# Optimization experiments

Measured on AMD Instinct MI355X. Metric: run time of the kernel, lower is better.

## Reference

```python
import jax, jax.numpy as jnp
import numpy as np

B, T, I, H, L, C = 8192, 50, 50, 10, 3, 5


def setup_inputs() -> dict:
    key = jax.random.key(0)
    ks = jax.random.split(key, 20)
    s = 1.0 / np.sqrt(H)  # torch nn.RNN init scale
    inp = {
        "x": jax.random.normal(ks[0], (B, T, I), dtype=jnp.float32),
        "h0": jax.random.normal(ks[1], (L, B, H), dtype=jnp.float32),
    }
    # per-layer weights: layer 0 takes input_size I, layers 1,2 take H
    in_sizes = [I, H, H]
    for l in range(L):
        inp[f"W_ih{l}"] = jax.random.uniform(ks[2 + 4 * l], (H, in_sizes[l]), minval=-s, maxval=s, dtype=jnp.float32)
        inp[f"W_hh{l}"] = jax.random.uniform(ks[3 + 4 * l], (H, H), minval=-s, maxval=s, dtype=jnp.float32)
        inp[f"b_ih{l}"] = jax.random.uniform(ks[4 + 4 * l], (H,), minval=-s, maxval=s, dtype=jnp.float32)
        inp[f"b_hh{l}"] = jax.random.uniform(ks[5 + 4 * l], (H,), minval=-s, maxval=s, dtype=jnp.float32)
    sf = 1.0 / np.sqrt(H * T)
    inp["fc_w"] = jax.random.uniform(ks[14], (C, H * T), minval=-sf, maxval=sf, dtype=jnp.float32)
    inp["fc_b"] = jax.random.uniform(ks[15], (C,), minval=-sf, maxval=sf, dtype=jnp.float32)
    return inp


def _rnn_layer(x, h0, W_ih, b_ih, W_hh, b_hh):
    # x: [B, T, in], h0: [B, H]. h_t = tanh(x_t W_ih^T + b_ih + h_{t-1} W_hh^T + b_hh)
    xW = jnp.einsum("bti,hi->bth", x, W_ih) + (b_ih + b_hh)  # input proj precomputed

    def step(h, xw_t):
        h = jnp.tanh(xw_t + h @ W_hh.T)
        return h, h

    _, ys = jax.lax.scan(step, h0, jnp.swapaxes(xW, 0, 1))  # ys: [T, B, H]
    return jnp.swapaxes(ys, 0, 1)  # [B, T, H]


def reference(x, h0, W_ih0, W_hh0, b_ih0, b_hh0, W_ih1, W_hh1, b_ih1, b_hh1,
              W_ih2, W_hh2, b_ih2, b_hh2, fc_w, fc_b):
    layers = [(W_ih0, b_ih0, W_hh0, b_hh0),
              (W_ih1, b_ih1, W_hh1, b_hh1),
              (W_ih2, b_ih2, W_hh2, b_hh2)]
    out = x
    for l, (Wi, bi, Wh, bh) in enumerate(layers):
        out = _rnn_layer(out, h0[l], Wi, bi, Wh, bh)
    flat = jax.nn.relu(out.reshape(out.shape[0], -1))  # [B, T*H]
    return flat @ fc_w.T + fc_b  # [B, C]
```

## Files before the change

### kernel.cpp

```cpp
#include <hip/hip_runtime.h>

#define BB 8192
#define TT 50
#define II 50
#define HH 10
#define CC 5

__device__ __forceinline__ float fast_tanh(float x) {
    float e = __expf(2.0f * x);
    return 1.0f - 2.0f * __builtin_amdgcn_rcpf(e + 1.0f);
}

#define SWZ(x, K) __uint_as_float((unsigned)__builtin_amdgcn_ds_swizzle( \
    (int)__float_as_uint(x), (((K) << 5) | 0x10)))
#define BC10(H, src)                                                     \
    H[0] = SWZ(src, 0); H[1] = SWZ(src, 1); H[2] = SWZ(src, 2);          \
    H[3] = SWZ(src, 3); H[4] = SWZ(src, 4); H[5] = SWZ(src, 5);          \
    H[6] = SWZ(src, 6); H[7] = SWZ(src, 7); H[8] = SWZ(src, 8);          \
    H[9] = SWZ(src, 9);

__global__ __launch_bounds__(256) void k_proj0(
    const float* __restrict__ x, const float* __restrict__ Wih0,
    const float* __restrict__ bih0, const float* __restrict__ bhh0,
    float* __restrict__ P) {
    int gid = blockIdx.x * 256 + threadIdx.x;
    int b = gid & (BB - 1);
    int t = gid >> 13;
    const float2* xr = (const float2*)(x + ((size_t)b * TT + t) * II);
    float2 xv[II / 2];
#pragma unroll
    for (int i = 0; i < II / 2; i++) xv[i] = xr[i];
#pragma unroll
    for (int j = 0; j < HH; j++) {
        float a = bih0[j] + bhh0[j];
        const float2* w = (const float2*)(Wih0 + j * II);
#pragma unroll
        for (int i = 0; i < II / 2; i++) {
            float2 wv = w[i];
            a = fmaf(wv.x, xv[i].x, a);
            a = fmaf(wv.y, xv[i].y, a);
        }
        P[((size_t)t * HH + j) * BB + b] = a;
    }
}

__global__ __launch_bounds__(256, 2) void k_fused(
    const float* __restrict__ h0all,
    const float* __restrict__ Whh0,
    const float* __restrict__ Wih1, const float* __restrict__ Whh1,
    const float* __restrict__ bih1, const float* __restrict__ bhh1,
    const float* __restrict__ Wih2, const float* __restrict__ Whh2,
    const float* __restrict__ bih2, const float* __restrict__ bhh2,
    const float* __restrict__ fcw, const float* __restrict__ fcb,
    const float* __restrict__ P, float* __restrict__ out) {
    __shared__ __align__(16) float sfc8[TT * HH * 8];

    const int tid = threadIdx.x;
    const int j = tid & 15;
    const int g16 = tid >> 4;
    const int b = blockIdx.x * 16 + g16;
    const bool jv = (j < HH);

    for (int idx = tid; idx < TT * HH * 8; idx += 256) {
        int r = idx >> 3, c = idx & 7;
        sfc8[idx] = (c < CC) ? fcw[(size_t)c * (TT * HH) + r] : 0.0f;
    }

    float w0[HH], wi1[HH], wh1[HH], wi2[HH], wh2[HH];
    float bs1 = 0.0f, bs2 = 0.0f, h1i = 0.0f, h2i = 0.0f, h0i = 0.0f;
    if (jv) {
#pragma unroll
        for (int k = 0; k < HH; k++) {
            w0[k]  = Whh0[j * HH + k];
            wi1[k] = Wih1[j * HH + k];
            wh1[k] = Whh1[j * HH + k];
            wi2[k] = Wih2[j * HH + k];
            wh2[k] = Whh2[j * HH + k];
        }
        bs1 = bih1[j] + bhh1[j];
        bs2 = bih2[j] + bhh2[j];
        h0i = h0all[(size_t)b * HH + j];
        h1i = h0all[(size_t)BB * HH + (size_t)b * HH + j];
        h2i = h0all[(size_t)2 * BB * HH + (size_t)b * HH + j];
    } else {
#pragma unroll
        for (int k = 0; k < HH; k++) {
            w0[k] = wi1[k] = wh1[k] = wi2[k] = wh2[k] = 0.0f;
        }
    }

    __syncthreads();

    float h0o = h0i, h1o = h1i, h2o = h2i;

    float acc[CC] = {0.0f, 0.0f, 0.0f, 0.0f, 0.0f};

    float p0 = jv ? P[(size_t)(0 * HH + j) * BB + b] : 0.0f;
    float p1 = jv ? P[(size_t)(1 * HH + j) * BB + b] : 0.0f;
    float p2 = jv ? P[(size_t)(2 * HH + j) * BB + b] : 0.0f;
    float p3 = jv ? P[(size_t)(3 * HH + j) * BB + b] : 0.0f;

#pragma unroll 1
    for (int i = 0; i < TT + 2; i++) {
        float H0[HH], H1[HH], H2[HH];
        BC10(H0, h0o)
        BC10(H1, h1o)
        BC10(H2, h2o)

        int tp = (i + 4 < TT) ? (i + 4) : (TT - 1);
        float pnew = jv ? P[(size_t)(tp * HH + j) * BB + b] : 0.0f;

        int tauc = (i >= 2) ? (i - 2) : 0;
        const float* fb = &sfc8[(tauc * HH + j) * 8];
        float4 f4 = *(const float4*)fb;
        float  f1 = fb[4];

        float a0 = p0, a1 = bs1, a2 = bs2;
#pragma unroll
        for (int k = 0; k < HH; k++) {
            a0 = fmaf(w0[k],  H0[k], a0);
            a1 = fmaf(wi1[k], H0[k], a1);
            a1 = fmaf(wh1[k], H1[k], a1);
            a2 = fmaf(wi2[k], H1[k], a2);
            a2 = fmaf(wh2[k], H2[k], a2);
        }
        float t0 = fast_tanh(a0);
        float t1 = fast_tanh(a1);
        float t2 = fast_tanh(a2);

        if (i >= 2 && jv) {
            float rl = fmaxf(t2, 0.0f);
            acc[0] = fmaf(f4.x, rl, acc[0]);
            acc[1] = fmaf(f4.y, rl, acc[1]);
            acc[2] = fmaf(f4.z, rl, acc[2]);
            acc[3] = fmaf(f4.w, rl, acc[3]);
            acc[4] = fmaf(f1,  rl, acc[4]);
        }

        h0o = t0;
        h1o = (i == 0) ? h1i : t1;
        h2o = (i <= 1) ? h2i : t2;
        p0 = p1; p1 = p2; p2 = p3; p3 = pnew;
    }

#pragma unroll
    for (int c = 0; c < CC; c++) {
        float a = acc[c];
        a += __shfl_xor(a, 1);
        a += __shfl_xor(a, 2);
        a += __shfl_xor(a, 4);
        a += __shfl_xor(a, 8);
        acc[c] = a + fcb[c];
    }
    if (j == 0) {
#pragma unroll
        for (int c = 0; c < CC; c++) out[(size_t)b * CC + c] = acc[c];
    }
}

extern "C" void kernel_launch(void* const* d_in, const int* in_sizes, int n_in,
                              void* d_out, int out_size, void* d_ws, size_t ws_size,
                              hipStream_t stream) {
    const float* x    = (const float*)d_in[0];
    const float* h0   = (const float*)d_in[1];
    const float* Wih0 = (const float*)d_in[2];
    const float* Whh0 = (const float*)d_in[3];
    const float* bih0 = (const float*)d_in[4];
    const float* bhh0 = (const float*)d_in[5];
    const float* Wih1 = (const float*)d_in[6];
    const float* Whh1 = (const float*)d_in[7];
    const float* bih1 = (const float*)d_in[8];
    const float* bhh1 = (const float*)d_in[9];
    const float* Wih2 = (const float*)d_in[10];
    const float* Whh2 = (const float*)d_in[11];
    const float* bih2 = (const float*)d_in[12];
    const float* bhh2 = (const float*)d_in[13];
    const float* fcw  = (const float*)d_in[14];
    const float* fcb  = (const float*)d_in[15];
    float* out = (float*)d_out;
    float* P   = (float*)d_ws;

    k_proj0<<<(BB * TT) / 256, 256, 0, stream>>>(x, Wih0, bih0, bhh0, P);
    k_fused<<<BB / 16, 256, 0, stream>>>(h0, Whh0, Wih1, Whh1, bih1, bhh1,
                                         Wih2, Whh2, bih2, bhh2, fcw, fcb, P, out);
}
```

Before: 64.15 us.

## Fuse input projection via bf16 MFMA into recurrence kernel with DPP row reductions

```diff
diff --git a/kernel.cpp b/kernel.cpp
--- a/kernel.cpp
+++ b/kernel.cpp
@@ -1,4 +1,5 @@
 #include <hip/hip_runtime.h>
+#include <hip/hip_bf16.h>
 
 #define BB 8192
 #define TT 50
@@ -6,141 +7,200 @@
 #define HH 10
 #define CC 5
 
+typedef __attribute__((ext_vector_type(8))) short short8;
+typedef __attribute__((ext_vector_type(4))) float f32x4;
+
+struct U4 { unsigned x, y, z, w; };
+__device__ __forceinline__ short8 toB(unsigned a, unsigned b, unsigned c, unsigned d) {
+    U4 u{a, b, c, d};
+    return __builtin_bit_cast(short8, u);
+}
+__device__ __forceinline__ unsigned short bfbits(float f) {
+    __hip_bfloat16 h = __float2bfloat16(f);
+    union { __hip_bfloat16 h; unsigned short u; } cv;
+    cv.h = h;
+    return cv.u;
+}
+__device__ __forceinline__ unsigned packbf(float a, float b) {
+    return ((unsigned)bfbits(b) << 16) | (unsigned)bfbits(a);
+}
+
 __device__ __forceinline__ float fast_tanh(float x) {
     float e = __expf(2.0f * x);
     return 1.0f - 2.0f * __builtin_amdgcn_rcpf(e + 1.0f);
 }
 
-#define SWZ(x, K) __uint_as_float((unsigned)__builtin_amdgcn_ds_swizzle( \
-    (int)__float_as_uint(x), (((K) << 5) | 0x10)))
-#define BC10(H, src)                                                     \
-    H[0] = SWZ(src, 0); H[1] = SWZ(src, 1); H[2] = SWZ(src, 2);          \
-    H[3] = SWZ(src, 3); H[4] = SWZ(src, 4); H[5] = SWZ(src, 5);          \
-    H[6] = SWZ(src, 6); H[7] = SWZ(src, 7); H[8] = SWZ(src, 8);          \
-    H[9] = SWZ(src, 9);
-
-__global__ __launch_bounds__(256) void k_proj0(
-    const float* __restrict__ x, const float* __restrict__ Wih0,
+__device__ __forceinline__ float ror_sum16(float v) {
+    unsigned u;
+    u = __builtin_amdgcn_update_dpp(0, (int)__float_as_uint(v), 0x121, 0xf, 0xf, false);
+    v += __uint_as_float(u);
+    u = __builtin_amdgcn_update_dpp(0, (int)__float_as_uint(v), 0x122, 0xf, 0xf, false);
+    v += __uint_as_float(u);
+    u = __builtin_amdgcn_update_dpp(0, (int)__float_as_uint(v), 0x124, 0xf, 0xf, false);
+    v += __uint_as_float(u);
+    u = __builtin_amdgcn_update_dpp(0, (int)__float_as_uint(v), 0x128, 0xf, 0xf, false);
+    v += __uint_as_float(u);
+    return v;
+}
+
+__global__ __launch_bounds__(256, 2) void k_all(
+    const float* __restrict__ x, const float* __restrict__ h0all,
+    const float* __restrict__ Wih0, const float* __restrict__ Whh0,
     const float* __restrict__ bih0, const float* __restrict__ bhh0,
-    float* __restrict__ P) {
-    int gid = blockIdx.x * 256 + threadIdx.x;
-    int b = gid & (BB - 1);
-    int t = gid >> 13;
-    const float2* xr = (const float2*)(x + ((size_t)b * TT + t) * II);
-    float2 xv[II / 2];
-#pragma unroll
-    for (int i = 0; i < II / 2; i++) xv[i] = xr[i];
-#pragma unroll
-    for (int j = 0; j < HH; j++) {
-        float a = bih0[j] + bhh0[j];
-        const float2* w = (const float2*)(Wih0 + j * II);
-#pragma unroll
-        for (int i = 0; i < II / 2; i++) {
-            float2 wv = w[i];
-            a = fmaf(wv.x, xv[i].x, a);
-            a = fmaf(wv.y, xv[i].y, a);
-        }
-        P[((size_t)t * HH + j) * BB + b] = a;
-    }
-}
-
-__global__ __launch_bounds__(256, 2) void k_fused(
-    const float* __restrict__ h0all,
-    const float* __restrict__ Whh0,
     const float* __restrict__ Wih1, const float* __restrict__ Whh1,
     const float* __restrict__ bih1, const float* __restrict__ bhh1,
     const float* __restrict__ Wih2, const float* __restrict__ Whh2,
     const float* __restrict__ bih2, const float* __restrict__ bhh2,
     const float* __restrict__ fcw, const float* __restrict__ fcb,
-    const float* __restrict__ P, float* __restrict__ out) {
+    float* __restrict__ out) {
+    __shared__ __align__(16) float sp[TT * 16 * 12];
     __shared__ __align__(16) float sfc8[TT * HH * 8];
 
     const int tid = threadIdx.x;
-    const int j = tid & 15;
-    const int g16 = tid >> 4;
-    const int b = blockIdx.x * 16 + g16;
-    const bool jv = (j < HH);
+    const int bb0 = blockIdx.x * 16;
 
     for (int idx = tid; idx < TT * HH * 8; idx += 256) {
         int r = idx >> 3, c = idx & 7;
         sfc8[idx] = (c < CC) ? fcw[(size_t)c * (TT * HH) + r] : 0.0f;
     }
 
-    float w0[HH], wi1[HH], wh1[HH], wi2[HH], wh2[HH];
+    {
+        const int w = tid >> 6;
+        const int lane = tid & 63;
+        const int bl = lane & 15;
+        const int g = lane >> 4;
+
+        short8 A0, A1;
+#pragma unroll
+        for (int e = 0; e < 8; e++) {
+            int k0 = g * 8 + e;
+            int k1 = 32 + g * 8 + e;
+            float v0 = (bl < HH) ? Wih0[bl * II + k0] : 0.0f;
+            float v1 = (bl < HH && k1 < II) ? Wih0[bl * II + k1] : 0.0f;
+            A0[e] = (short)bfbits(v0);
+            A1[e] = (short)bfbits(v1);
+        }
+        f32x4 bc;
+#pragma unroll
+        for (int r = 0; r < 4; r++) {
+            int j = g * 4 + r;
+            bc[r] = (j < HH) ? (bih0[j] + bhh0[j]) : 0.0f;
+        }
+
+#pragma unroll 1
+        for (int tt = 0; tt < 13; tt++) {
+            int t = w * 13 + tt;
+            if (t < TT) {
+                const float* xb = x + (size_t)(bb0 + bl) * (TT * II) + t * II;
+                float2 q0 = *(const float2*)(xb + g * 8);
+                float2 q1 = *(const float2*)(xb + g * 8 + 2);
+                float2 q2 = *(const float2*)(xb + g * 8 + 4);
+                float2 q3 = *(const float2*)(xb + g * 8 + 6);
+                short8 B0 = toB(packbf(q0.x, q0.y), packbf(q1.x, q1.y),
+                                packbf(q2.x, q2.y), packbf(q3.x, q3.y));
+                float xv[8] = {0.f, 0.f, 0.f, 0.f, 0.f, 0.f, 0.f, 0.f};
+                if (g < 2) {
+                    float2 a = *(const float2*)(xb + 32 + g * 8);
+                    float2 b2 = *(const float2*)(xb + 34 + g * 8);
+                    float2 c = *(const float2*)(xb + 36 + g * 8);
+                    float2 d = *(const float2*)(xb + 38 + g * 8);
+                    xv[0] = a.x; xv[1] = a.y; xv[2] = b2.x; xv[3] = b2.y;
+                    xv[4] = c.x; xv[5] = c.y; xv[6] = d.x; xv[7] = d.y;
+                } else if (g == 2) {
+                    float2 a = *(const float2*)(xb + 48);
+                    xv[0] = a.x; xv[1] = a.y;
+                }
+                short8 B1 = toB(packbf(xv[0], xv[1]), packbf(xv[2], xv[3]),
+                                packbf(xv[4], xv[5]), packbf(xv[6], xv[7]));
+                f32x4 D = __builtin_amdgcn_mfma_f32_16x16x32_bf16(A0, B0, bc, 0, 0, 0);
+                D = __builtin_amdgcn_mfma_f32_16x16x32_bf16(A1, B1, D, 0, 0, 0);
+                if (g < 3) {
+                    float* dst = &sp[(t * 16 + bl) * 12 + g * 4];
+                    float2 d01; d01.x = D[0]; d01.y = D[1];
+                    float2 d23; d23.x = D[2]; d23.y = D[3];
+                    *(float2*)dst = d01;
+                    *(float2*)(dst + 2) = d23;
+                }
+            }
+        }
+    }
+
+    const int k = tid & 15;
+    const int g16 = tid >> 4;
+    const int b = bb0 + g16;
+    const bool kv = (k < HH);
+
+    float w0c[HH], wi1c[HH], wh1c[HH], wi2c[HH], wh2c[HH], sel[HH];
     float bs1 = 0.0f, bs2 = 0.0f, h1i = 0.0f, h2i = 0.0f, h0i = 0.0f;
-    if (jv) {
-#pragma unroll
-        for (int k = 0; k < HH; k++) {
-            w0[k]  = Whh0[j * HH + k];
-            wi1[k] = Wih1[j * HH + k];
-            wh1[k] = Whh1[j * HH + k];
-            wi2[k] = Wih2[j * HH + k];
-            wh2[k] = Whh2[j * HH + k];
-        }
-        bs1 = bih1[j] + bhh1[j];
-        bs2 = bih2[j] + bhh2[j];
-        h0i = h0all[(size_t)b * HH + j];
-        h1i = h0all[(size_t)BB * HH + (size_t)b * HH + j];
-        h2i = h0all[(size_t)2 * BB * HH + (size_t)b * HH + j];
-    } else {
-#pragma unroll
-        for (int k = 0; k < HH; k++) {
-            w0[k] = wi1[k] = wh1[k] = wi2[k] = wh2[k] = 0.0f;
-        }
-    }
+#pragma unroll
+    for (int j = 0; j < HH; j++) {
+        w0c[j]  = kv ? Whh0[j * HH + k] : 0.0f;
+        wi1c[j] = kv ? Wih1[j * HH + k] : 0.0f;
+        wh1c[j] = kv ? Whh1[j * HH + k] : 0.0f;
+        wi2c[j] = kv ? Wih2[j * HH + k] : 0.0f;
+        wh2c[j] = kv ? Whh2[j * HH + k] : 0.0f;
+        sel[j] = (k == j) ? 1.0f : 0.0f;
+    }
+    if (kv) {
+        bs1 = bih1[k] + bhh1[k];
+        bs2 = bih2[k] + bhh2[k];
+        h0i = h0all[(size_t)b * HH + k];
+        h1i = h0all[(size_t)BB * HH + (size_t)b * HH + k];
+        h2i = h0all[(size_t)2 * BB * HH + (size_t)b * HH + k];
+    }
+    float h0 = h0i, h1 = h1i, h2 = h2i;
+    float acc[CC] = {0.0f, 0.0f, 0.0f, 0.0f, 0.0f};
 
     __syncthreads();
 
-    float h0o = h0i, h1o = h1i, h2o = h2i;
-
-    float acc[CC] = {0.0f, 0.0f, 0.0f, 0.0f, 0.0f};
-
-    float p0 = jv ? P[(size_t)(0 * HH + j) * BB + b] : 0.0f;
-    float p1 = jv ? P[(size_t)(1 * HH + j) * BB + b] : 0.0f;
-    float p2 = jv ? P[(size_t)(2 * HH + j) * BB + b] : 0.0f;
-    float p3 = jv ? P[(size_t)(3 * HH + j) * BB + b] : 0.0f;
+    float pcur = kv ? sp[(0 * 16 + g16) * 12 + k] : 0.0f;
 
 #pragma unroll 1
     for (int i = 0; i < TT + 2; i++) {
-        float H0[HH], H1[HH], H2[HH];
-        BC10(H0, h0o)
-        BC10(H1, h1o)
-        BC10(H2, h2o)
-
-        int tp = (i + 4 < TT) ? (i + 4) : (TT - 1);
-        float pnew = jv ? P[(size_t)(tp * HH + j) * BB + b] : 0.0f;
-
+        int tp = (i + 1 < TT) ? (i + 1) : (TT - 1);
+        float pn = kv ? sp[(tp * 16 + g16) * 12 + k] : 0.0f;
         int tauc = (i >= 2) ? (i - 2) : 0;
-        const float* fb = &sfc8[(tauc * HH + j) * 8];
-        float4 f4 = *(const float4*)fb;
-        float  f1 = fb[4];
-
-        float a0 = p0, a1 = bs1, a2 = bs2;
-#pragma unroll
-        for (int k = 0; k < HH; k++) {
-            a0 = fmaf(w0[k],  H0[k], a0);
-            a1 = fmaf(wi1[k], H0[k], a1);
-            a1 = fmaf(wh1[k], H1[k], a1);
-            a2 = fmaf(wi2[k], H1[k], a2);
-            a2 = fmaf(wh2[k], H2[k], a2);
-        }
+        float4 f4v = {0.f, 0.f, 0.f, 0.f};
+        float f1v = 0.0f;
+        if (kv) {
+            const float* fb = &sfc8[(tauc * HH + k) * 8];
+            f4v = *(const float4*)fb;
+            f1v = fb[4];
+        }
+
+        float r[HH];
+#pragma unroll
+        for (int j = 0; j < HH; j++) r[j] = ror_sum16(w0c[j] * h0);
+        float a0 = pcur;
+#pragma unroll
+        for (int j = 0; j < HH; j++) a0 = fmaf(sel[j], r[j], a0);
         float t0 = fast_tanh(a0);
+#pragma unroll
+        for (int j = 0; j < HH; j++) r[j] = ror_sum16(fmaf(wh1c[j], h1, wi1c[j] * h0));
+        float a1 = bs1;
+#pragma unroll
+        for (int j = 0; j < HH; j++) a1 = fmaf(sel[j], r[j], a1);
         float t1 = fast_tanh(a1);
+#pragma unroll
+        for (int j = 0; j < HH; j++) r[j] = ror_sum16(fmaf(wh2c[j], h2, wi2c[j] * h1));
+        float a2 = bs2;
+#pragma unroll
+        for (int j = 0; j < HH; j++) a2 = fmaf(sel[j], r[j], a2);
         float t2 = fast_tanh(a2);
 
-        if (i >= 2 && jv) {
+        if (i >= 2 && kv) {
             float rl = fmaxf(t2, 0.0f);
-            acc[0] = fmaf(f4.x, rl, acc[0]);
-            acc[1] = fmaf(f4.y, rl, acc[1]);
-            acc[2] = fmaf(f4.z, rl, acc[2]);
-            acc[3] = fmaf(f4.w, rl, acc[3]);
-            acc[4] = fmaf(f1,  rl, acc[4]);
-        }
-
-        h0o = t0;
-        h1o = (i == 0) ? h1i : t1;
-        h2o = (i <= 1) ? h2i : t2;
-        p0 = p1; p1 = p2; p2 = p3; p3 = pnew;
+            acc[0] = fmaf(f4v.x, rl, acc[0]);
+            acc[1] = fmaf(f4v.y, rl, acc[1]);
+            acc[2] = fmaf(f4v.z, rl, acc[2]);
+            acc[3] = fmaf(f4v.w, rl, acc[3]);
+            acc[4] = fmaf(f1v,  rl, acc[4]);
+        }
+
+        h0 = t0;
+        h1 = (i == 0) ? h1i : t1;
+        h2 = (i <= 1) ? h2i : t2;
+        pcur = pn;
     }
 
 #pragma unroll
@@ -152,7 +212,7 @@
         a += __shfl_xor(a, 8);
         acc[c] = a + fcb[c];
     }
-    if (j == 0) {
+    if (k == 0) {
 #pragma unroll
         for (int c = 0; c < CC; c++) out[(size_t)b * CC + c] = acc[c];
     }
@@ -178,9 +238,8 @@
     const float* fcw  = (const float*)d_in[14];
     const float* fcb  = (const float*)d_in[15];
     float* out = (float*)d_out;
-    float* P   = (float*)d_ws;
-
-    k_proj0<<<(BB * TT) / 256, 256, 0, stream>>>(x, Wih0, bih0, bhh0, P);
-    k_fused<<<BB / 16, 256, 0, stream>>>(h0, Whh0, Wih1, Whh1, bih1, bhh1,
-                                         Wih2, Whh2, bih2, bhh2, fcw, fcb, P, out);
-}
+
+    k_all<<<BB / 16, 256, 0, stream>>>(x, h0, Wih0, Whh0, bih0, bhh0,
+                                       Wih1, Whh1, bih1, bhh1,
+                                       Wih2, Whh2, bih2, bhh2, fcw, fcb, out);
+}
```

After: 78.49 us. 1.22x slower.

## Replace ds_swizzle broadcasts with DPP row-rotate ring matvec

Applied to the files above, without the earlier changes.

```diff
diff --git a/kernel.cpp b/kernel.cpp
--- a/kernel.cpp
+++ b/kernel.cpp
@@ -11,13 +11,13 @@
     return 1.0f - 2.0f * __builtin_amdgcn_rcpf(e + 1.0f);
 }
 
-#define SWZ(x, K) __uint_as_float((unsigned)__builtin_amdgcn_ds_swizzle( \
-    (int)__float_as_uint(x), (((K) << 5) | 0x10)))
-#define BC10(H, src)                                                     \
-    H[0] = SWZ(src, 0); H[1] = SWZ(src, 1); H[2] = SWZ(src, 2);          \
-    H[3] = SWZ(src, 3); H[4] = SWZ(src, 4); H[5] = SWZ(src, 5);          \
-    H[6] = SWZ(src, 6); H[7] = SWZ(src, 7); H[8] = SWZ(src, 8);          \
-    H[9] = SWZ(src, 9);
+__device__ __forceinline__ float rot1(float v) {
+    return __uint_as_float((unsigned)__builtin_amdgcn_update_dpp(
+        0, (int)__float_as_uint(v), 0x121 , 0xF, 0xF, false));
+}
+__device__ __forceinline__ int rot1_i(int v) {
+    return __builtin_amdgcn_update_dpp(0, v, 0x121, 0xF, 0xF, false);
+}
 
 __global__ __launch_bounds__(256) void k_proj0(
     const float* __restrict__ x, const float* __restrict__ Wih0,
@@ -53,7 +53,7 @@
     const float* __restrict__ bih2, const float* __restrict__ bhh2,
     const float* __restrict__ fcw, const float* __restrict__ fcb,
     const float* __restrict__ P, float* __restrict__ out) {
-    __shared__ __align__(16) float sfc8[TT * HH * 8];
+    __shared__ __align__(16) float sfc8[(TT * HH + 8) * 8];
 
     const int tid = threadIdx.x;
     const int j = tid & 15;
@@ -65,70 +65,70 @@
         int r = idx >> 3, c = idx & 7;
         sfc8[idx] = (c < CC) ? fcw[(size_t)c * (TT * HH) + r] : 0.0f;
     }
+    for (int idx = TT * HH * 8 + tid; idx < (TT * HH + 8) * 8; idx += 256)
+        sfc8[idx] = 0.0f;
 
-    float w0[HH], wi1[HH], wh1[HH], wi2[HH], wh2[HH];
-    float bs1 = 0.0f, bs2 = 0.0f, h1i = 0.0f, h2i = 0.0f, h0i = 0.0f;
+    const int q = rot1_i(j) & 15;
+    const bool dplus = (q == ((j + 1) & 15));
+
+    float w0s[16], wi1s[16], wh1s[16], wi2s[16], wh2s[16];
+#pragma unroll
+    for (int r = 0; r < 16; r++) {
+        int k = dplus ? ((j + r) & 15) : ((j - r) & 15);
+        bool v = jv && (k < HH);
+        float a = 0.f, bw = 0.f, c = 0.f, d = 0.f, e = 0.f;
+        if (v) {
+            a = Whh0[j * HH + k];
+            bw = Wih1[j * HH + k];
+            c = Whh1[j * HH + k];
+            d = Wih2[j * HH + k];
+            e = Whh2[j * HH + k];
+        }
+        w0s[r] = a; wi1s[r] = bw; wh1s[r] = c; wi2s[r] = d; wh2s[r] = e;
+    }
+    float bs1 = 0.0f, bs2 = 0.0f, h0i = 0.0f, h1i = 0.0f, h2i = 0.0f;
     if (jv) {
-#pragma unroll
-        for (int k = 0; k < HH; k++) {
-            w0[k]  = Whh0[j * HH + k];
-            wi1[k] = Wih1[j * HH + k];
-            wh1[k] = Whh1[j * HH + k];
-            wi2[k] = Wih2[j * HH + k];
-            wh2[k] = Whh2[j * HH + k];
-        }
         bs1 = bih1[j] + bhh1[j];
         bs2 = bih2[j] + bhh2[j];
         h0i = h0all[(size_t)b * HH + j];
         h1i = h0all[(size_t)BB * HH + (size_t)b * HH + j];
         h2i = h0all[(size_t)2 * BB * HH + (size_t)b * HH + j];
-    } else {
-#pragma unroll
-        for (int k = 0; k < HH; k++) {
-            w0[k] = wi1[k] = wh1[k] = wi2[k] = wh2[k] = 0.0f;
-        }
     }
 
     __syncthreads();
 
-    float h0o = h0i, h1o = h1i, h2o = h2i;
-
+    float h0 = h0i, h1 = h1i, h2 = h2i;
     float acc[CC] = {0.0f, 0.0f, 0.0f, 0.0f, 0.0f};
 
-    float p0 = jv ? P[(size_t)(0 * HH + j) * BB + b] : 0.0f;
+    float pc = jv ? P[(size_t)j * BB + b] : 0.0f;
     float p1 = jv ? P[(size_t)(1 * HH + j) * BB + b] : 0.0f;
-    float p2 = jv ? P[(size_t)(2 * HH + j) * BB + b] : 0.0f;
-    float p3 = jv ? P[(size_t)(3 * HH + j) * BB + b] : 0.0f;
 
 #pragma unroll 1
     for (int i = 0; i < TT + 2; i++) {
-        float H0[HH], H1[HH], H2[HH];
-        BC10(H0, h0o)
-        BC10(H1, h1o)
-        BC10(H2, h2o)
-
-        int tp = (i + 4 < TT) ? (i + 4) : (TT - 1);
-        float pnew = jv ? P[(size_t)(tp * HH + j) * BB + b] : 0.0f;
+        int tp = (i + 2 < TT) ? (i + 2) : (TT - 1);
+        float p2 = jv ? P[(size_t)(tp * HH + j) * BB + b] : 0.0f;
 
         int tauc = (i >= 2) ? (i - 2) : 0;
         const float* fb = &sfc8[(tauc * HH + j) * 8];
         float4 f4 = *(const float4*)fb;
         float  f1 = fb[4];
 
-        float a0 = p0, a1 = bs1, a2 = bs2;
+        float a0 = pc, a1 = bs1, a2 = bs2;
+        float r0 = h0, r1 = h1, r2 = h2;
 #pragma unroll
-        for (int k = 0; k < HH; k++) {
-            a0 = fmaf(w0[k],  H0[k], a0);
-            a1 = fmaf(wi1[k], H0[k], a1);
-            a1 = fmaf(wh1[k], H1[k], a1);
-            a2 = fmaf(wi2[k], H1[k], a2);
-            a2 = fmaf(wh2[k], H2[k], a2);
+        for (int r = 0; r < 16; r++) {
+            a0 = fmaf(w0s[r],  r0, a0);
+            a1 = fmaf(wi1s[r], r0, a1);
+            a1 = fmaf(wh1s[r], r1, a1);
+            a2 = fmaf(wi2s[r], r1, a2);
+            a2 = fmaf(wh2s[r], r2, a2);
+            if (r < 15) { r0 = rot1(r0); r1 = rot1(r1); r2 = rot1(r2); }
         }
         float t0 = fast_tanh(a0);
         float t1 = fast_tanh(a1);
         float t2 = fast_tanh(a2);
 
-        if (i >= 2 && jv) {
+        if (i >= 2) {
             float rl = fmaxf(t2, 0.0f);
             acc[0] = fmaf(f4.x, rl, acc[0]);
             acc[1] = fmaf(f4.y, rl, acc[1]);
@@ -137,10 +137,11 @@
             acc[4] = fmaf(f1,  rl, acc[4]);
         }
 
-        h0o = t0;
-        h1o = (i == 0) ? h1i : t1;
-        h2o = (i <= 1) ? h2i : t2;
-        p0 = p1; p1 = p2; p2 = p3; p3 = pnew;
+        h0 = t0;
+        h1 = (i == 0) ? h1i : t1;
+        h2 = (i <= 1) ? h2i : t2;
+        pc = p1;
+        p1 = p2;
     }
 
 #pragma unroll
```

Result: slower. 74.19 us (+15.6%).

## Broadcast hidden states through double-buffered LDS as packed bf16 pairs

Applied to the files above, without the earlier changes.

```diff
diff --git a/kernel.cpp b/kernel.cpp
--- a/kernel.cpp
+++ b/kernel.cpp
@@ -1,4 +1,5 @@
 #include <hip/hip_runtime.h>
+#include <hip/hip_bf16.h>
 
 #define BB 8192
 #define TT 50
@@ -10,14 +11,20 @@
     float e = __expf(2.0f * x);
     return 1.0f - 2.0f * __builtin_amdgcn_rcpf(e + 1.0f);
 }
-
-#define SWZ(x, K) __uint_as_float((unsigned)__builtin_amdgcn_ds_swizzle( \
-    (int)__float_as_uint(x), (((K) << 5) | 0x10)))
-#define BC10(H, src)                                                     \
-    H[0] = SWZ(src, 0); H[1] = SWZ(src, 1); H[2] = SWZ(src, 2);          \
-    H[3] = SWZ(src, 3); H[4] = SWZ(src, 4); H[5] = SWZ(src, 5);          \
-    H[6] = SWZ(src, 6); H[7] = SWZ(src, 7); H[8] = SWZ(src, 8);          \
-    H[9] = SWZ(src, 9);
+__device__ __forceinline__ unsigned short bfbits(float f) {
+    __hip_bfloat16 h = __float2bfloat16(f);
+    union { __hip_bfloat16 h; unsigned short u; } cv;
+    cv.h = h;
+    return cv.u;
+}
+__device__ __forceinline__ unsigned packbf(float a, float b) {
+    return ((unsigned)bfbits(b) << 16) | (unsigned)bfbits(a);
+}
+__device__ __forceinline__ float qswap1(float x) {
+    return __uint_as_float((unsigned)__builtin_amdgcn_update_dpp(
+        (int)__float_as_uint(x), (int)__float_as_uint(x), 0xB1, 0xF, 0xF, true));
+}
+#define UNPK(d, e, o) { unsigned _d = (d); e = __uint_as_float(_d << 16); o = __uint_as_float(_d & 0xFFFF0000u); }
 
 __global__ __launch_bounds__(256) void k_proj0(
     const float* __restrict__ x, const float* __restrict__ Wih0,
@@ -53,21 +60,23 @@
     const float* __restrict__ bih2, const float* __restrict__ bhh2,
     const float* __restrict__ fcw, const float* __restrict__ fcb,
     const float* __restrict__ P, float* __restrict__ out) {
-    __shared__ __align__(16) float sfc8[TT * HH * 8];
+    __shared__ __align__(16) float sfc8[(TT * HH + 8) * 8];
+    __shared__ __align__(16) unsigned shp[2][16][5][4];
 
     const int tid = threadIdx.x;
     const int j = tid & 15;
     const int g16 = tid >> 4;
     const int b = blockIdx.x * 16 + g16;
     const bool jv = (j < HH);
-
-    for (int idx = tid; idx < TT * HH * 8; idx += 256) {
+    const bool wr = jv && !(j & 1);
+
+    for (int idx = tid; idx < (TT * HH + 8) * 8; idx += 256) {
         int r = idx >> 3, c = idx & 7;
-        sfc8[idx] = (c < CC) ? fcw[(size_t)c * (TT * HH) + r] : 0.0f;
+        sfc8[idx] = (r < TT * HH && c < CC) ? fcw[(size_t)c * (TT * HH) + r] : 0.0f;
     }
 
     float w0[HH], wi1[HH], wh1[HH], wi2[HH], wh2[HH];
-    float bs1 = 0.0f, bs2 = 0.0f, h1i = 0.0f, h2i = 0.0f, h0i = 0.0f;
+    float bs1 = 0.0f, bs2 = 0.0f, h0i = 0.0f, h1i = 0.0f, h2i = 0.0f;
     if (jv) {
 #pragma unroll
         for (int k = 0; k < HH; k++) {
@@ -89,33 +98,54 @@
         }
     }
 
+    {
+        float p0 = qswap1(h0i), p1 = qswap1(h1i), p2 = qswap1(h2i);
+        if (wr) {
+            uint4 wv;
+            wv.x = packbf(h0i, p0);
+            wv.y = packbf(h1i, p1);
+            wv.z = packbf(h2i, p2);
+            wv.w = 0u;
+            *(uint4*)&shp[1][g16][j >> 1][0] = wv;
+        }
+    }
+
     __syncthreads();
 
-    float h0o = h0i, h1o = h1i, h2o = h2i;
-
     float acc[CC] = {0.0f, 0.0f, 0.0f, 0.0f, 0.0f};
 
-    float p0 = jv ? P[(size_t)(0 * HH + j) * BB + b] : 0.0f;
-    float p1 = jv ? P[(size_t)(1 * HH + j) * BB + b] : 0.0f;
-    float p2 = jv ? P[(size_t)(2 * HH + j) * BB + b] : 0.0f;
-    float p3 = jv ? P[(size_t)(3 * HH + j) * BB + b] : 0.0f;
+    const float* Pb = P + (size_t)j * BB + b;
+    float pc = jv ? Pb[(size_t)0 * HH * BB] : 0.0f;
+    float p1 = jv ? Pb[(size_t)1 * HH * BB] : 0.0f;
+    float p2 = jv ? Pb[(size_t)2 * HH * BB] : 0.0f;
+
+    const unsigned* shR = &shp[1][g16][0][0];
+    unsigned*       shW = &shp[0][g16][0][0];
 
 #pragma unroll 1
     for (int i = 0; i < TT + 2; i++) {
-        float H0[HH], H1[HH], H2[HH];
-        BC10(H0, h0o)
-        BC10(H1, h1o)
-        BC10(H2, h2o)
-
-        int tp = (i + 4 < TT) ? (i + 4) : (TT - 1);
-        float pnew = jv ? P[(size_t)(tp * HH + j) * BB + b] : 0.0f;
+        uint4 q0 = *(const uint4*)(shR + 0);
+        uint4 q1 = *(const uint4*)(shR + 4);
+        uint4 q2 = *(const uint4*)(shR + 8);
+        uint4 q3 = *(const uint4*)(shR + 12);
+        uint4 q4 = *(const uint4*)(shR + 16);
+
+        int tp = (i + 3 < TT) ? (i + 3) : (TT - 1);
+        float p3 = jv ? Pb[(size_t)tp * HH * BB] : 0.0f;
 
         int tauc = (i >= 2) ? (i - 2) : 0;
         const float* fb = &sfc8[(tauc * HH + j) * 8];
         float4 f4 = *(const float4*)fb;
         float  f1 = fb[4];
 
-        float a0 = p0, a1 = bs1, a2 = bs2;
+        float H0[HH], H1[HH], H2[HH];
+        UNPK(q0.x, H0[0], H0[1]) UNPK(q0.y, H1[0], H1[1]) UNPK(q0.z, H2[0], H2[1])
+        UNPK(q1.x, H0[2], H0[3]) UNPK(q1.y, H1[2], H1[3]) UNPK(q1.z, H2[2], H2[3])
+        UNPK(q2.x, H0[4], H0[5]) UNPK(q2.y, H1[4], H1[5]) UNPK(q2.z, H2[4], H2[5])
+        UNPK(q3.x, H0[6], H0[7]) UNPK(q3.y, H1[6], H1[7]) UNPK(q3.z, H2[6], H2[7])
+        UNPK(q4.x, H0[8], H0[9]) UNPK(q4.y, H1[8], H1[9]) UNPK(q4.z, H2[8], H2[9])
+
+        float a0 = pc, a1 = bs1, a2 = bs2;
 #pragma unroll
         for (int k = 0; k < HH; k++) {
             a0 = fmaf(w0[k],  H0[k], a0);
@@ -137,10 +167,20 @@
             acc[4] = fmaf(f1,  rl, acc[4]);
         }
 
-        h0o = t0;
-        h1o = (i == 0) ? h1i : t1;
-        h2o = (i <= 1) ? h2i : t2;
-        p0 = p1; p1 = p2; p2 = p3; p3 = pnew;
+        float v0 = t0;
+        float v1 = (i == 0) ? h1i : t1;
+        float v2 = (i <= 1) ? h2i : t2;
+        float o0 = qswap1(v0), o1 = qswap1(v1), o2 = qswap1(v2);
+        if (wr) {
+            uint4 wv;
+            wv.x = packbf(v0, o0);
+            wv.y = packbf(v1, o1);
+            wv.z = packbf(v2, o2);
+            wv.w = 0u;
+            *(uint4*)(shW + (j >> 1) * 4) = wv;
+        }
+        unsigned* tmp = (unsigned*)shR; shR = shW; shW = tmp;
+        pc = p1; p1 = p2; p2 = p3;
     }
 
 #pragma unroll
```

Result: slower. 68.40 us (+6.6%).
